# Optimization experiments

Measured on AMD Instinct MI355X. Metric: run time of the kernel, lower is better.

## Reference

```python
import jax, jax.numpy as jnp
import numpy as np

N_QUBITS = 4


def _apply_rx(state, theta, wire):
    # state: [B, 2,2,2,2] complex64, theta: [B] real angles; RX on `wire`.
    st = jnp.moveaxis(state, wire + 1, -1)
    bshape = (theta.shape[0],) + (1,) * (st.ndim - 2)
    c = jnp.cos(theta * 0.5).reshape(bshape).astype(jnp.complex64)
    s = (-1j) * jnp.sin(theta * 0.5).reshape(bshape).astype(jnp.complex64)
    new = jnp.stack([c * st[..., 0] + s * st[..., 1],
                     s * st[..., 0] + c * st[..., 1]], axis=-1)
    return jnp.moveaxis(new, -1, wire + 1)


def _apply_cnot(state, control, target):
    st = jnp.moveaxis(state, (control + 1, target + 1), (-2, -1))
    new = jnp.stack([st[..., 0, :], st[..., 1, ::-1]], axis=-2)
    return jnp.moveaxis(new, (-2, -1), (control + 1, target + 1))


def _quantum_gate(angles, thetas):
    # angles: [B, n] data-encoding RX angles; thetas: [n] trainable RX angles.
    B, n = angles.shape
    state = jnp.zeros((B,) + (2,) * n, jnp.complex64)
    state = state.at[(slice(None),) + (0,) * n].set(1.0)  # |0...0>
    for w in range(n):
        state = _apply_rx(state, angles[:, w], w)
    for w in range(n):
        state = _apply_rx(state, jnp.broadcast_to(thetas[w], (B,)), w)
    for w in range(n):
        state = _apply_cnot(state, w, (w + 1) % n)
    probs = jnp.abs(state.reshape(B, 2 ** n)) ** 2  # [B, 16]
    bits = (np.arange(2 ** n)[:, None] >> np.arange(n - 1, -1, -1)[None, :]) & 1
    signs = jnp.asarray(1.0 - 2.0 * bits, jnp.float32)  # [16, n] PauliZ eigvals
    return probs @ signs  # [B, n] <Z_w> expectations


def setup_inputs() -> dict:
    key = jax.random.key(0)
    ks = jax.random.split(key, 12)
    B, D, H, n = 131072, 256, 4, N_QUBITS
    fan_in = D + H
    sc = 1.0 / np.sqrt(fan_in)
    inp = {
        'x': jax.random.normal(ks[0], (B, D), jnp.float32),
        'hx': jax.random.normal(ks[1], (B, H), jnp.float32),
        'cx': jax.random.normal(ks[2], (B, H), jnp.float32),
        'W_f': jax.random.normal(ks[3], (n, fan_in), jnp.float32) * sc,
        'b_f': jnp.zeros((n,), jnp.float32),
        'W_i': jax.random.normal(ks[4], (n, fan_in), jnp.float32) * sc,
        'b_i': jnp.zeros((n,), jnp.float32),
        'W_u': jax.random.normal(ks[5], (n, fan_in), jnp.float32) * sc,
        'b_u': jnp.zeros((n,), jnp.float32),
        'W_o': jax.random.normal(ks[6], (n, fan_in), jnp.float32) * sc,
        'b_o': jnp.zeros((n,), jnp.float32),
        'th_f': jax.random.normal(ks[7], (n,), jnp.float32),
        'th_i': jax.random.normal(ks[8], (n,), jnp.float32),
        'th_u': jax.random.normal(ks[9], (n,), jnp.float32),
        'th_o': jax.random.normal(ks[10], (n,), jnp.float32),
    }
    return inp


def reference(x, hx, cx, W_f, b_f, W_i, b_i, W_u, b_u, W_o, b_o,
              th_f, th_i, th_u, th_o):
    comb = jnp.concatenate([x, hx], axis=1)  # [B, D+H]
    f = jax.nn.sigmoid(_quantum_gate(comb @ W_f.T + b_f, th_f))
    i = jax.nn.sigmoid(_quantum_gate(comb @ W_i.T + b_i, th_i))
    g = jnp.tanh(_quantum_gate(comb @ W_u.T + b_u, th_u))
    o = jax.nn.sigmoid(_quantum_gate(comb @ W_o.T + b_o, th_o))
    c_new = f * cx + i * g
    h_new = o * jnp.tanh(c_new)
    return (h_new, c_new)
```

## Files before the change

kernel.cpp:

```cpp
#include <hip/hip_runtime.h>

#define NB   131072
#define TPB  128
#define FANIN 260

__device__ __forceinline__ float sigm_(float x) { return 1.0f / (1.0f + __expf(-x)); }
__device__ __forceinline__ float tanh_(float x) { return 1.0f - 2.0f / (__expf(2.0f * x) + 1.0f); }

__global__ void qlstm_prep(const float* __restrict__ Wf, const float* __restrict__ bf,
                           const float* __restrict__ Wi, const float* __restrict__ bi,
                           const float* __restrict__ Wu, const float* __restrict__ bu,
                           const float* __restrict__ Wo, const float* __restrict__ bo,
                           const float* __restrict__ thf, const float* __restrict__ thi,
                           const float* __restrict__ thu, const float* __restrict__ tho,
                           float* __restrict__ Wp, float* __restrict__ bth) {
    int t = blockIdx.x * blockDim.x + threadIdx.x;
    if (t < FANIN * 16) {
        int k = t >> 4, gw = t & 15, g = gw >> 2, w = gw & 3;
        const float* Wg = (g == 0) ? Wf : (g == 1) ? Wi : (g == 2) ? Wu : Wo;
        Wp[t] = Wg[w * FANIN + k];
    }
    if (t < 16) {
        int g = t >> 2, w = t & 3;
        const float* bg = (g == 0) ? bf  : (g == 1) ? bi  : (g == 2) ? bu  : bo;
        const float* tg = (g == 0) ? thf : (g == 1) ? thi : (g == 2) ? thu : tho;
        bth[t] = bg[w] + tg[w];
    }
}

__global__ __launch_bounds__(TPB) void qlstm_main(
        const float* __restrict__ x, const float* __restrict__ hx,
        const float* __restrict__ cx, const float* __restrict__ Wp,
        const float* __restrict__ bth, float* __restrict__ out) {
    __shared__ float xs[TPB * 33];

    const int tid  = threadIdx.x;
    const int row0 = blockIdx.x * TPB;
    const int row  = row0 + tid;

    float4 hv  = ((const float4*)hx)[row];
    float4 cxv = ((const float4*)cx)[row];

    float acc[16];
#pragma unroll
    for (int j = 0; j < 16; ++j) acc[j] = 0.0f;

    const float4* x4 = (const float4*)x;

    float4 pre[8];
#pragma unroll
    for (int u = 0; u < 8; ++u) {
        int f = tid + (u << 7);
        pre[u] = x4[(size_t)(row0 + (f >> 3)) * 64 + (f & 7)];
    }

    for (int stage = 0; stage < 8; ++stage) {
#pragma unroll
        for (int u = 0; u < 8; ++u) {
            int f = tid + (u << 7);
            float* dst = &xs[(f >> 3) * 33 + ((f & 7) << 2)];
            dst[0] = pre[u].x; dst[1] = pre[u].y; dst[2] = pre[u].z; dst[3] = pre[u].w;
        }
        __syncthreads();

        if (stage < 7) {
#pragma unroll
            for (int u = 0; u < 8; ++u) {
                int f = tid + (u << 7);
                pre[u] = x4[(size_t)(row0 + (f >> 3)) * 64 + (stage + 1) * 8 + (f & 7)];
            }
        }

        const float* xrow  = &xs[tid * 33];
        const float* wbase = Wp + stage * 32 * 16;
#pragma unroll
        for (int kk = 0; kk < 32; ++kk) {
            float xv = xrow[kk];
            const float* wp = wbase + kk * 16;
#pragma unroll
            for (int j = 0; j < 16; ++j) acc[j] = fmaf(xv, wp[j], acc[j]);
        }
        __syncthreads();
    }

    {
        const float* wp = Wp + 256 * 16;
#pragma unroll
        for (int j = 0; j < 16; ++j) acc[j] = fmaf(hv.x, wp[j],      acc[j]);
#pragma unroll
        for (int j = 0; j < 16; ++j) acc[j] = fmaf(hv.y, wp[16 + j], acc[j]);
#pragma unroll
        for (int j = 0; j < 16; ++j) acc[j] = fmaf(hv.z, wp[32 + j], acc[j]);
#pragma unroll
        for (int j = 0; j < 16; ++j) acc[j] = fmaf(hv.w, wp[48 + j], acc[j]);
    }

    float co[16];
#pragma unroll
    for (int j = 0; j < 16; ++j) co[j] = __cosf(acc[j] + bth[j]);

    float G[16];
#pragma unroll
    for (int g = 0; g < 4; ++g) {
        float c0 = co[g * 4 + 0], c1 = co[g * 4 + 1];
        float c2 = co[g * 4 + 2], c3 = co[g * 4 + 3];
        float e1 = c0 * c1;
        float e2 = e1 * c2;
        float e3 = e2 * c3;
        float e0 = c1 * c2 * c3;
        G[g * 4 + 0] = e0; G[g * 4 + 1] = e1; G[g * 4 + 2] = e2; G[g * 4 + 3] = e3;
    }

    float cxa[4] = {cxv.x, cxv.y, cxv.z, cxv.w};

    float hn[4], cn[4];
#pragma unroll
    for (int w = 0; w < 4; ++w) {
        float fg = sigm_(G[0 * 4 + w]);
        float ig = sigm_(G[1 * 4 + w]);
        float ug = tanh_(G[2 * 4 + w]);
        float og = sigm_(G[3 * 4 + w]);
        float c_ = fg * cxa[w] + ig * ug;
        cn[w] = c_;
        hn[w] = og * tanh_(c_);
    }

    ((float4*)out)[row]      = make_float4(hn[0], hn[1], hn[2], hn[3]);
    ((float4*)out)[NB + row] = make_float4(cn[0], cn[1], cn[2], cn[3]);
}

extern "C" void kernel_launch(void* const* d_in, const int* in_sizes, int n_in,
                              void* d_out, int out_size, void* d_ws, size_t ws_size,
                              hipStream_t stream) {
    const float* x   = (const float*)d_in[0];
    const float* hx  = (const float*)d_in[1];
    const float* cx  = (const float*)d_in[2];
    const float* Wf  = (const float*)d_in[3];
    const float* bf  = (const float*)d_in[4];
    const float* Wi  = (const float*)d_in[5];
    const float* bi  = (const float*)d_in[6];
    const float* Wu  = (const float*)d_in[7];
    const float* bu  = (const float*)d_in[8];
    const float* Wo  = (const float*)d_in[9];
    const float* bo  = (const float*)d_in[10];
    const float* thf = (const float*)d_in[11];
    const float* thi = (const float*)d_in[12];
    const float* thu = (const float*)d_in[13];
    const float* tho = (const float*)d_in[14];

    float* Wp  = (float*)d_ws;
    float* bth = Wp + FANIN * 16;

    qlstm_prep<<<(FANIN * 16 + 255) / 256, 256, 0, stream>>>(
        Wf, bf, Wi, bi, Wu, bu, Wo, bo, thf, thi, thu, tho, Wp, bth);

    qlstm_main<<<NB / TPB, TPB, 0, stream>>>(
        x, hx, cx, Wp, bth, (float*)d_out);
}
```

Baseline: 228.8 us.

## Split K-reduction across four waves per row block with shared-memory combine

Each block now handles 64 rows with 256 threads. The four wavefronts each take an 8-column slice of every 32-wide x tile, so every thread does a quarter of the dot-product work. Partial 16-wide accumulators from waves 1-3 are written to shared memory and summed by wave 0, which then runs the cosine, gate and LSTM epilogue and writes the outputs. This doubles the number of blocks and cuts per-thread prefetch registers to raise occupancy and latency hiding. The cost is an extra shared-memory reduction and barrier, and three of the four waves sit idle during the epilogue.

```diff
diff --git a/kernel.cpp b/kernel.cpp
--- a/kernel.cpp
+++ b/kernel.cpp
@@ -1,8 +1,11 @@
 #include <hip/hip_runtime.h>
 
-#define NB   131072
-#define TPB  128
-#define FANIN 260
+#define NB      131072
+#define TPB     256
+#define RPB     64
+#define FANIN   260
+#define XSTRIDE 34
+#define PSTRIDE 17
 
 __device__ __forceinline__ float sigm_(float x) { return 1.0f / (1.0f + __expf(-x)); }
 __device__ __forceinline__ float tanh_(float x) { return 1.0f - 2.0f / (__expf(2.0f * x) + 1.0f); }
@@ -28,62 +31,67 @@
     }
 }
 
-__global__ __launch_bounds__(TPB) void qlstm_main(
+__global__ __launch_bounds__(TPB, 8) void qlstm_main(
         const float* __restrict__ x, const float* __restrict__ hx,
         const float* __restrict__ cx, const float* __restrict__ Wp,
         const float* __restrict__ bth, float* __restrict__ out) {
-    __shared__ float xs[TPB * 33];
+    __shared__ float smem[3 * RPB * PSTRIDE];
 
     const int tid  = threadIdx.x;
-    const int row0 = blockIdx.x * TPB;
-    const int row  = row0 + tid;
+    const int row0 = blockIdx.x * RPB;
+    const int r    = tid & 63;
+    const int w    = __builtin_amdgcn_readfirstlane(tid >> 6);
 
-    float4 hv  = ((const float4*)hx)[row];
-    float4 cxv = ((const float4*)cx)[row];
+    const float4* x4 = (const float4*)x;
+
+    float4 hv  = make_float4(0.f, 0.f, 0.f, 0.f);
+    float4 cxv = make_float4(0.f, 0.f, 0.f, 0.f);
+    if (w == 3) hv  = ((const float4*)hx)[row0 + r];
+    if (w == 0) cxv = ((const float4*)cx)[row0 + r];
+
+    const int r_st = tid >> 3;
+    const int c4   = tid & 7;
+
+    float4 pre[2];
+#pragma unroll
+    for (int u = 0; u < 2; ++u)
+        pre[u] = x4[(size_t)(row0 + r_st + 32 * u) * 64 + c4];
 
     float acc[16];
 #pragma unroll
     for (int j = 0; j < 16; ++j) acc[j] = 0.0f;
 
-    const float4* x4 = (const float4*)x;
-
-    float4 pre[8];
-#pragma unroll
-    for (int u = 0; u < 8; ++u) {
-        int f = tid + (u << 7);
-        pre[u] = x4[(size_t)(row0 + (f >> 3)) * 64 + (f & 7)];
-    }
+    const float* xrow = &smem[r * XSTRIDE + (w << 3)];
 
     for (int stage = 0; stage < 8; ++stage) {
 #pragma unroll
-        for (int u = 0; u < 8; ++u) {
-            int f = tid + (u << 7);
-            float* dst = &xs[(f >> 3) * 33 + ((f & 7) << 2)];
-            dst[0] = pre[u].x; dst[1] = pre[u].y; dst[2] = pre[u].z; dst[3] = pre[u].w;
+        for (int u = 0; u < 2; ++u) {
+            float* dst = &smem[(r_st + 32 * u) * XSTRIDE + (c4 << 2)];
+            *(float2*)(dst)     = make_float2(pre[u].x, pre[u].y);
+            *(float2*)(dst + 2) = make_float2(pre[u].z, pre[u].w);
         }
         __syncthreads();
 
         if (stage < 7) {
 #pragma unroll
-            for (int u = 0; u < 8; ++u) {
-                int f = tid + (u << 7);
-                pre[u] = x4[(size_t)(row0 + (f >> 3)) * 64 + (stage + 1) * 8 + (f & 7)];
-            }
+            for (int u = 0; u < 2; ++u)
+                pre[u] = x4[(size_t)(row0 + r_st + 32 * u) * 64 + ((stage + 1) << 3) + c4];
         }
 
-        const float* xrow  = &xs[tid * 33];
-        const float* wbase = Wp + stage * 32 * 16;
+        const float* wbase = Wp + (((stage << 5) + (w << 3)) << 4);
 #pragma unroll
-        for (int kk = 0; kk < 32; ++kk) {
-            float xv = xrow[kk];
-            const float* wp = wbase + kk * 16;
+        for (int k2 = 0; k2 < 4; ++k2) {
+            float2 xv = *(const float2*)(xrow + (k2 << 1));
+            const float* wp0 = wbase + (k2 << 5);
 #pragma unroll
-            for (int j = 0; j < 16; ++j) acc[j] = fmaf(xv, wp[j], acc[j]);
+            for (int j = 0; j < 16; ++j) acc[j] = fmaf(xv.x, wp0[j],      acc[j]);
+#pragma unroll
+            for (int j = 0; j < 16; ++j) acc[j] = fmaf(xv.y, wp0[16 + j], acc[j]);
         }
         __syncthreads();
     }
 
-    {
+    if (w == 3) {
         const float* wp = Wp + 256 * 16;
 #pragma unroll
         for (int j = 0; j < 16; ++j) acc[j] = fmaf(hv.x, wp[j],      acc[j]);
@@ -95,38 +103,53 @@
         for (int j = 0; j < 16; ++j) acc[j] = fmaf(hv.w, wp[48 + j], acc[j]);
     }
 
-    float co[16];
+    if (w > 0) {
+        float* p = &smem[(w - 1) * (RPB * PSTRIDE) + r * PSTRIDE];
 #pragma unroll
-    for (int j = 0; j < 16; ++j) co[j] = __cosf(acc[j] + bth[j]);
+        for (int j = 0; j < 16; ++j) p[j] = acc[j];
+    }
+    __syncthreads();
 
-    float G[16];
+    if (w == 0) {
 #pragma unroll
-    for (int g = 0; g < 4; ++g) {
-        float c0 = co[g * 4 + 0], c1 = co[g * 4 + 1];
-        float c2 = co[g * 4 + 2], c3 = co[g * 4 + 3];
-        float e1 = c0 * c1;
-        float e2 = e1 * c2;
-        float e3 = e2 * c3;
-        float e0 = c1 * c2 * c3;
-        G[g * 4 + 0] = e0; G[g * 4 + 1] = e1; G[g * 4 + 2] = e2; G[g * 4 + 3] = e3;
+        for (int wm = 0; wm < 3; ++wm) {
+            const float* p = &smem[wm * (RPB * PSTRIDE) + r * PSTRIDE];
+#pragma unroll
+            for (int j = 0; j < 16; ++j) acc[j] += p[j];
+        }
+
+        float co[16];
+#pragma unroll
+        for (int j = 0; j < 16; ++j) co[j] = __cosf(acc[j] + bth[j]);
+
+        float G[16];
+#pragma unroll
+        for (int g = 0; g < 4; ++g) {
+            float c0 = co[g * 4 + 0], c1 = co[g * 4 + 1];
+            float c2 = co[g * 4 + 2], c3 = co[g * 4 + 3];
+            float e1 = c0 * c1;
+            float e2 = e1 * c2;
+            float e3 = e2 * c3;
+            float e0 = c1 * c2 * c3;
+            G[g * 4 + 0] = e0; G[g * 4 + 1] = e1; G[g * 4 + 2] = e2; G[g * 4 + 3] = e3;
+        }
+
+        float cxa[4] = {cxv.x, cxv.y, cxv.z, cxv.w};
+        float hn[4], cn[4];
+#pragma unroll
+        for (int wi = 0; wi < 4; ++wi) {
+            float fg = sigm_(G[0 * 4 + wi]);
+            float ig = sigm_(G[1 * 4 + wi]);
+            float ug = tanh_(G[2 * 4 + wi]);
+            float og = sigm_(G[3 * 4 + wi]);
+            float c_ = fg * cxa[wi] + ig * ug;
+            cn[wi] = c_;
+            hn[wi] = og * tanh_(c_);
+        }
+
+        ((float4*)out)[row0 + r]      = make_float4(hn[0], hn[1], hn[2], hn[3]);
+        ((float4*)out)[NB + row0 + r] = make_float4(cn[0], cn[1], cn[2], cn[3]);
     }
-
-    float cxa[4] = {cxv.x, cxv.y, cxv.z, cxv.w};
-
-    float hn[4], cn[4];
-#pragma unroll
-    for (int w = 0; w < 4; ++w) {
-        float fg = sigm_(G[0 * 4 + w]);
-        float ig = sigm_(G[1 * 4 + w]);
-        float ug = tanh_(G[2 * 4 + w]);
-        float og = sigm_(G[3 * 4 + w]);
-        float c_ = fg * cxa[w] + ig * ug;
-        cn[w] = c_;
-        hn[w] = og * tanh_(c_);
-    }
-
-    ((float4*)out)[row]      = make_float4(hn[0], hn[1], hn[2], hn[3]);
-    ((float4*)out)[NB + row] = make_float4(cn[0], cn[1], cn[2], cn[3]);
 }
 
 extern "C" void kernel_launch(void* const* d_in, const int* in_sizes, int n_in,
@@ -154,6 +177,6 @@
     qlstm_prep<<<(FANIN * 16 + 255) / 256, 256, 0, stream>>>(
         Wf, bf, Wi, bi, Wu, bu, Wo, bo, thf, thi, thu, tho, Wp, bth);
 
-    qlstm_main<<<NB / TPB, TPB, 0, stream>>>(
+    qlstm_main<<<NB / RPB, TPB, 0, stream>>>(
         x, hx, cx, Wp, bth, (float*)d_out);
 }
```

New measurement: 226.3 us. No clear change (-1.1%).
